# Kernel tuning notes

Measured on AMD Instinct MI355X. Metric: run time of the kernel, lower is better.

Reference implementation:

```python
import jax, jax.numpy as jnp
import numpy as np


def setup_inputs() -> dict:
    key = jax.random.key(0)
    ks = jax.random.split(key, 8)
    B, N, M = 8, 4096, 4096
    return {
        "R": jax.random.normal(ks[0], (B, 3, 3), dtype=jnp.float32),
        "t": jax.random.normal(ks[1], (B, 3), dtype=jnp.float32),
        "S": jax.random.uniform(ks[2], (B,), dtype=jnp.float32),
        "R_g": jax.random.normal(ks[3], (B, 3, 3), dtype=jnp.float32),
        "t_g": jax.random.normal(ks[4], (B, 3), dtype=jnp.float32),
        "S_g": jax.random.uniform(ks[5], (B,), dtype=jnp.float32),
        "T_X": jax.random.normal(ks[6], (B, N, 3), dtype=jnp.float32),
        "Y": jax.random.normal(ks[7], (B, M, 3), dtype=jnp.float32),
    }


def _chamfer(x, y):
    # x: [B,N,3], y: [B,M,3]. Pairwise Euclidean distances [B,N,M] via the
    x2 = jnp.sum(x * x, axis=-1)                      # [B,N]
    y2 = jnp.sum(y * y, axis=-1)                      # [B,M]
    xy = jnp.einsum('bnd,bmd->bnm', x, y)             # [B,N,M]
    d2 = x2[:, :, None] + y2[:, None, :] - 2.0 * xy
    dist = jnp.sqrt(jnp.maximum(d2, 0.0))             # [B,N,M]
    min_x_to_y = jnp.min(dist, axis=2)                # [B,N]
    min_y_to_x = jnp.min(dist, axis=1)                # [B,M]
    per_batch = jnp.mean(min_x_to_y, axis=1) + jnp.mean(min_y_to_x, axis=1)
    return jnp.mean(per_batch)


def _registration(R, t, S, R_g, t_g, S_g):
    eye = jnp.eye(3, dtype=R.dtype)
    diff = jnp.einsum('bji,bjk->bik', R_g, R) - eye   # R_g^T @ R - I, [B,3,3]
    L_R = jnp.sum(diff * diff, axis=(1, 2))           # squared Frobenius norm
    L_t = jnp.sum((t_g - t) ** 2, axis=1)
    L_S = (S_g - S) ** 2
    return jnp.mean(L_R + L_t + L_S)


def reference(R, t, S, R_g, t_g, S_g, T_X, Y):
    L_R = _registration(R, t, S, R_g, t_g, S_g)
    L_CD = _chamfer(T_X, Y)
    return (L_R + L_CD, L_R, L_CD)
```

## Files before the change

kernel.cpp:

```cpp
#include <hip/hip_runtime.h>
#include <hip/hip_bf16.h>

constexpr int B_ = 8;
constexpr int N_ = 4096;
constexpr int M_ = 4096;
constexpr int TPB = 256;
constexpr int HALF_PTS = 2048;
constexpr int NTILE = HALF_PTS / 16;
constexpr int NQ = 2 * B_ * N_;

typedef _Float16 half8 __attribute__((ext_vector_type(8)));
typedef float    f32x4 __attribute__((ext_vector_type(4)));

__global__ __launch_bounds__(TPB) void chamfer_mfma(
    const float* __restrict__ X, const float* __restrict__ Yp,
    float* __restrict__ part, float* __restrict__ out)
{
    __shared__ half8 sB[HALF_PTS + 1];

    if (blockIdx.x == 0 && threadIdx.x < 3) out[threadIdx.x] = 0.0f;

    int bid = blockIdx.x;
    const int dir    = bid & 1;   bid >>= 1;
    const int half_  = bid & 1;   bid >>= 1;
    const int qchunk = bid & 15;  bid >>= 4;
    const int b      = bid;

    const float* q  = dir ? Yp : X;
    const float* db = dir ? X  : Yp;

    const int tid  = threadIdx.x;
    const int lane = tid & 63;
    const int wave = tid >> 6;
    const int l15  = lane & 15;

    const int dbbase = b * M_ + half_ * HALF_PTS;
    #pragma unroll
    for (int k = 0; k < 8; ++k) {
        const int pt = tid + k * TPB;
        const float* pp = db + (size_t)(dbbase + pt) * 3;
        float px = pp[0], py = pp[1], pz = pp[2];
        float pn = px * px + py * py + pz * pz;
        half8 v;
        v[0] = (_Float16)(-2.0f * px);
        v[1] = (_Float16)(-2.0f * py);
        v[2] = (_Float16)(-2.0f * pz);
        v[3] = (_Float16)pn;
        v[4] = (_Float16)0.0f; v[5] = (_Float16)0.0f;
        v[6] = (_Float16)0.0f; v[7] = (_Float16)0.0f;
        sB[pt] = v;
    }
    if (tid == 0) {
        half8 z;
        #pragma unroll
        for (int i = 0; i < 8; ++i) z[i] = (_Float16)0.0f;
        sB[HALF_PTS] = z;
    }

    const int qglob = b * N_ + qchunk * 256 + wave * 64;
    half8 af[4];
    #pragma unroll
    for (int f = 0; f < 4; ++f) {
        half8 v;
        #pragma unroll
        for (int i = 0; i < 8; ++i) v[i] = (_Float16)0.0f;
        if (lane < 16) {
            const float* qp = q + (size_t)(qglob + f * 16 + l15) * 3;
            v[0] = (_Float16)qp[0];
            v[1] = (_Float16)qp[1];
            v[2] = (_Float16)qp[2];
            v[3] = (_Float16)1.0f;
        }
        af[f] = v;
    }
    __syncthreads();

    const half8* bp = sB + ((lane < 16) ? l15 : HALF_PTS);
    const int step  = (lane < 16) ? 16 : 0;

    f32x4 zero4; zero4[0] = 0.f; zero4[1] = 0.f; zero4[2] = 0.f; zero4[3] = 0.f;
    const float BIG = 3.0e38f;
    float rm[4][4];
    #pragma unroll
    for (int f = 0; f < 4; ++f)
        #pragma unroll
        for (int i = 0; i < 4; ++i) rm[f][i] = BIG;

    for (int t = 0; t < NTILE; t += 2) {
        half8 b0 = bp[0];
        half8 b1 = bp[step];
        bp += (step << 1);
        f32x4 a0[4], a1[4];
        #pragma unroll
        for (int f = 0; f < 4; ++f)
            a0[f] = __builtin_amdgcn_mfma_f32_16x16x32_f16(af[f], b0, zero4, 0, 0, 0);
        #pragma unroll
        for (int f = 0; f < 4; ++f)
            a1[f] = __builtin_amdgcn_mfma_f32_16x16x32_f16(af[f], b1, zero4, 0, 0, 0);
        #pragma unroll
        for (int f = 0; f < 4; ++f)
            #pragma unroll
            for (int i = 0; i < 4; ++i)
                rm[f][i] = fminf(rm[f][i], fminf(a0[f][i], a1[f][i]));
    }

    #pragma unroll
    for (int f = 0; f < 4; ++f)
        #pragma unroll
        for (int i = 0; i < 4; ++i) {
            float v = rm[f][i];
            v = fminf(v, __shfl_xor(v, 1, 64));
            v = fminf(v, __shfl_xor(v, 2, 64));
            v = fminf(v, __shfl_xor(v, 4, 64));
            v = fminf(v, __shfl_xor(v, 8, 64));
            rm[f][i] = v;
        }

    const int f_sel = (lane >> 2) & 3;
    const int i_sel = lane & 3;
    float v = BIG;
    #pragma unroll
    for (int f = 0; f < 4; ++f)
        #pragma unroll
        for (int i = 0; i < 4; ++i)
            if (f == f_sel && i == i_sel) v = rm[f][i];

    const int j  = f_sel * 16 + ((lane >> 4) << 2) + i_sel;
    const int qs = qchunk * 256 + wave * 64 + j;
    const float* qp = q + (size_t)(b * N_ + qs) * 3;
    const float qn = qp[0] * qp[0] + qp[1] * qp[1] + qp[2] * qp[2];
    const float d2 = fmaxf(v + qn, 0.0f);
    part[half_ * NQ + dir * (B_ * N_) + b * N_ + qs] = d2;
}

__global__ __launch_bounds__(TPB) void finalize_fused(
    const float* __restrict__ part,
    const float* __restrict__ R,  const float* __restrict__ t,
    const float* __restrict__ S,  const float* __restrict__ Rg,
    const float* __restrict__ tg, const float* __restrict__ Sg,
    float* __restrict__ out)
{
    __shared__ float wsum[TPB / 64];
    __shared__ float sreg[8];
    const int tid = threadIdx.x;
    const int qid = blockIdx.x * TPB + tid;

    float m = fminf(part[qid], part[NQ + qid]);
    float d = sqrtf(m);

    #pragma unroll
    for (int off = 32; off > 0; off >>= 1) d += __shfl_down(d, off, 64);
    if ((tid & 63) == 0) wsum[tid >> 6] = d;

    if (blockIdx.x == 0 && tid < 8) {
        const float* Rb  = R  + tid * 9;
        const float* Rgb = Rg + tid * 9;
        float acc = 0.0f;
        #pragma unroll
        for (int i = 0; i < 3; ++i) {
            #pragma unroll
            for (int k = 0; k < 3; ++k) {
                float v = 0.0f;
                #pragma unroll
                for (int jj = 0; jj < 3; ++jj)
                    v = fmaf(Rgb[jj * 3 + i], Rb[jj * 3 + k], v);
                if (i == k) v -= 1.0f;
                acc = fmaf(v, v, acc);
            }
        }
        #pragma unroll
        for (int dd = 0; dd < 3; ++dd) {
            float dv = tg[tid * 3 + dd] - t[tid * 3 + dd];
            acc = fmaf(dv, dv, acc);
        }
        float dS = Sg[tid] - S[tid];
        acc = fmaf(dS, dS, acc);
        sreg[tid] = acc;
    }
    __syncthreads();

    if (tid == 0) {
        float bs = (wsum[0] + wsum[1] + wsum[2] + wsum[3]) * (1.0f / (B_ * N_));
        atomicAdd(&out[0], bs);
        atomicAdd(&out[2], bs);
        if (blockIdx.x == 0) {
            float rs = 0.0f;
            #pragma unroll
            for (int bb = 0; bb < 8; ++bb) rs += sreg[bb];
            float L_R = rs * (1.0f / B_);
            atomicAdd(&out[0], L_R);
            atomicAdd(&out[1], L_R);
        }
    }
}

extern "C" void kernel_launch(void* const* d_in, const int* in_sizes, int n_in,
                              void* d_out, int out_size, void* d_ws, size_t ws_size,
                              hipStream_t stream) {
    const float* R  = (const float*)d_in[0];
    const float* t  = (const float*)d_in[1];
    const float* S  = (const float*)d_in[2];
    const float* Rg = (const float*)d_in[3];
    const float* tg = (const float*)d_in[4];
    const float* Sg = (const float*)d_in[5];
    const float* X  = (const float*)d_in[6];
    const float* Yp = (const float*)d_in[7];
    float* out = (float*)d_out;

    float* part = (float*)d_ws;

    chamfer_mfma<<<2 * 2 * 16 * B_, TPB, 0, stream>>>(X, Yp, part, out);
    finalize_fused<<<NQ / TPB, TPB, 0, stream>>>(part, R, t, S, Rg, tg, Sg, out);
}
```

Measured before the change: 93.53 us.

## Fuse min-combine and per-query reduction into 1024-thread chamfer blocks

Each chamfer block now uses 1024 threads, loads the whole 4096-point database into LDS, and splits it into four quarters scanned by separate wave groups. The four partial minima are combined in shared memory, and the block does the sqrt and sum itself, writing one partial per block. The finalize step becomes a single block that sums 256 partials and writes the outputs directly without atomics. This removes the large per-query partial buffer round trip and the multi-block atomic reduction. The cost is 4x the LDS per block (about 68KB) and fewer, larger blocks (256 instead of 512), which lowers occupancy and parallelism.

```diff
diff --git a/kernel.cpp b/kernel.cpp
--- a/kernel.cpp
+++ b/kernel.cpp
@@ -4,25 +4,25 @@
 constexpr int B_ = 8;
 constexpr int N_ = 4096;
 constexpr int M_ = 4096;
-constexpr int TPB = 256;
-constexpr int HALF_PTS = 2048;
-constexpr int NTILE = HALF_PTS / 16;
-constexpr int NQ = 2 * B_ * N_;
+constexpr int TPB1 = 1024;
+constexpr int QPB = 256;
+constexpr int QUARTER = M_ / 4;
+constexpr int NTILE = QUARTER / 16;
+constexpr int NBLK = 2 * B_ * (N_ / QPB);
 
 typedef _Float16 half8 __attribute__((ext_vector_type(8)));
 typedef float    f32x4 __attribute__((ext_vector_type(4)));
 
-__global__ __launch_bounds__(TPB) void chamfer_mfma(
+__global__ __launch_bounds__(TPB1) void chamfer_fused(
     const float* __restrict__ X, const float* __restrict__ Yp,
-    float* __restrict__ part, float* __restrict__ out)
+    float* __restrict__ part)
 {
-    __shared__ half8 sB[HALF_PTS + 1];
-
-    if (blockIdx.x == 0 && threadIdx.x < 3) out[threadIdx.x] = 0.0f;
+    __shared__ half8 sB[M_ + 1];
+    __shared__ float smin[4 * QPB];
+    __shared__ float wsum16[16];
 
     int bid = blockIdx.x;
     const int dir    = bid & 1;   bid >>= 1;
-    const int half_  = bid & 1;   bid >>= 1;
     const int qchunk = bid & 15;  bid >>= 4;
     const int b      = bid;
 
@@ -32,12 +32,14 @@
     const int tid  = threadIdx.x;
     const int lane = tid & 63;
     const int wave = tid >> 6;
+    const int quarter = wave & 3;
+    const int qgroup  = wave >> 2;
     const int l15  = lane & 15;
 
-    const int dbbase = b * M_ + half_ * HALF_PTS;
-    #pragma unroll
-    for (int k = 0; k < 8; ++k) {
-        const int pt = tid + k * TPB;
+    const int dbbase = b * M_;
+    #pragma unroll
+    for (int k = 0; k < M_ / TPB1; ++k) {
+        const int pt = tid + k * TPB1;
         const float* pp = db + (size_t)(dbbase + pt) * 3;
         float px = pp[0], py = pp[1], pz = pp[2];
         float pn = px * px + py * py + pz * pz;
@@ -54,10 +56,10 @@
         half8 z;
         #pragma unroll
         for (int i = 0; i < 8; ++i) z[i] = (_Float16)0.0f;
-        sB[HALF_PTS] = z;
-    }
-
-    const int qglob = b * N_ + qchunk * 256 + wave * 64;
+        sB[M_] = z;
+    }
+
+    const int qglob = b * N_ + qchunk * QPB + qgroup * 64;
     half8 af[4];
     #pragma unroll
     for (int f = 0; f < 4; ++f) {
@@ -75,7 +77,7 @@
     }
     __syncthreads();
 
-    const half8* bp = sB + ((lane < 16) ? l15 : HALF_PTS);
+    const half8* bp = sB + ((lane < 16) ? (quarter * QUARTER + l15) : M_);
     const int step  = (lane < 16) ? 16 : 0;
 
     f32x4 zero4; zero4[0] = 0.f; zero4[1] = 0.f; zero4[2] = 0.f; zero4[3] = 0.f;
@@ -125,34 +127,47 @@
         for (int i = 0; i < 4; ++i)
             if (f == f_sel && i == i_sel) v = rm[f][i];
 
-    const int j  = f_sel * 16 + ((lane >> 4) << 2) + i_sel;
-    const int qs = qchunk * 256 + wave * 64 + j;
-    const float* qp = q + (size_t)(b * N_ + qs) * 3;
-    const float qn = qp[0] * qp[0] + qp[1] * qp[1] + qp[2] * qp[2];
-    const float d2 = fmaxf(v + qn, 0.0f);
-    part[half_ * NQ + dir * (B_ * N_) + b * N_ + qs] = d2;
+    const int j = f_sel * 16 + ((lane >> 4) << 2) + i_sel;
+    smin[quarter * QPB + qgroup * 64 + j] = v;
+    __syncthreads();
+
+    float d = 0.0f;
+    if (tid < QPB) {
+        float m = fminf(fminf(smin[tid], smin[QPB + tid]),
+                        fminf(smin[2 * QPB + tid], smin[3 * QPB + tid]));
+        const float* qp = q + (size_t)(b * N_ + qchunk * QPB + tid) * 3;
+        const float qn = qp[0] * qp[0] + qp[1] * qp[1] + qp[2] * qp[2];
+        d = sqrtf(fmaxf(m + qn, 0.0f));
+    }
+    #pragma unroll
+    for (int off = 32; off > 0; off >>= 1) d += __shfl_down(d, off, 64);
+    if (lane == 0) wsum16[wave] = d;
+    __syncthreads();
+    if (tid == 0) {
+        float s = 0.0f;
+        #pragma unroll
+        for (int w = 0; w < 16; ++w) s += wsum16[w];
+        part[blockIdx.x] = s;
+    }
 }
 
-__global__ __launch_bounds__(TPB) void finalize_fused(
+__global__ __launch_bounds__(256) void final_kernel(
     const float* __restrict__ part,
     const float* __restrict__ R,  const float* __restrict__ t,
     const float* __restrict__ S,  const float* __restrict__ Rg,
     const float* __restrict__ tg, const float* __restrict__ Sg,
     float* __restrict__ out)
 {
-    __shared__ float wsum[TPB / 64];
+    __shared__ float wsum[4];
     __shared__ float sreg[8];
     const int tid = threadIdx.x;
-    const int qid = blockIdx.x * TPB + tid;
-
-    float m = fminf(part[qid], part[NQ + qid]);
-    float d = sqrtf(m);
-
-    #pragma unroll
-    for (int off = 32; off > 0; off >>= 1) d += __shfl_down(d, off, 64);
-    if ((tid & 63) == 0) wsum[tid >> 6] = d;
-
-    if (blockIdx.x == 0 && tid < 8) {
+
+    float s = part[tid];
+    #pragma unroll
+    for (int off = 32; off > 0; off >>= 1) s += __shfl_down(s, off, 64);
+    if ((tid & 63) == 0) wsum[tid >> 6] = s;
+
+    if (tid < 8) {
         const float* Rb  = R  + tid * 9;
         const float* Rgb = Rg + tid * 9;
         float acc = 0.0f;
@@ -180,17 +195,15 @@
     __syncthreads();
 
     if (tid == 0) {
-        float bs = (wsum[0] + wsum[1] + wsum[2] + wsum[3]) * (1.0f / (B_ * N_));
-        atomicAdd(&out[0], bs);
-        atomicAdd(&out[2], bs);
-        if (blockIdx.x == 0) {
-            float rs = 0.0f;
-            #pragma unroll
-            for (int bb = 0; bb < 8; ++bb) rs += sreg[bb];
-            float L_R = rs * (1.0f / B_);
-            atomicAdd(&out[0], L_R);
-            atomicAdd(&out[1], L_R);
-        }
+        float tot = wsum[0] + wsum[1] + wsum[2] + wsum[3];
+        float L_CD = tot / (float)(B_ * N_);
+        float rs = 0.0f;
+        #pragma unroll
+        for (int bb = 0; bb < 8; ++bb) rs += sreg[bb];
+        float L_R = rs / (float)B_;
+        out[0] = L_R + L_CD;
+        out[1] = L_R;
+        out[2] = L_CD;
     }
 }
 
@@ -209,6 +222,6 @@
 
     float* part = (float*)d_ws;
 
-    chamfer_mfma<<<2 * 2 * 16 * B_, TPB, 0, stream>>>(X, Yp, part, out);
-    finalize_fused<<<NQ / TPB, TPB, 0, stream>>>(part, R, t, S, Rg, tg, Sg, out);
+    chamfer_fused<<<NBLK, TPB1, 0, stream>>>(X, Yp, part);
+    final_kernel<<<1, 256, 0, stream>>>(part, R, t, S, Rg, tg, Sg, out);
 }
```

New measurement: 82.40 us, median of 2. 11.9% less time.
